# Kernel optimization log

Measured on AMD Instinct MI355X. Metric: run time of the kernel, lower is better.

## Reference

```python
import jax, jax.numpy as jnp
import numpy as np

BETA = 0.9
THR = 1.0
ALPHA = 2.0  # snntorch ATan surrogate default

@jax.custom_vjp
def spike(x):
    # Heaviside spike with ATan surrogate gradient (snntorch default)
    return (x > 0).astype(x.dtype)

def _spike_fwd(x):
    return spike(x), x

def _spike_bwd(x, g):
    grad = (ALPHA / 2.0) / (1.0 + (jnp.pi / 2.0 * ALPHA * x) ** 2)
    return (g * grad,)

spike.defvjp(_spike_fwd, _spike_bwd)

def setup_inputs() -> dict:
    key = jax.random.key(0)
    k1, k2, k3 = jax.random.split(key, 3)
    T, B, NI, NH, NO = 250, 256, 700, 1024, 20
    input_spikes = (jax.random.uniform(k1, (T, B, NI)) < 0.1).astype(jnp.float32)
    W1 = jax.random.normal(k2, (NH, NI), dtype=jnp.float32) / np.float32(np.sqrt(NI))
    W2 = jax.random.normal(k3, (NO, NH), dtype=jnp.float32) / np.float32(np.sqrt(NH))
    return {"input_spikes": input_spikes, "W1": W1, "W2": W2}

def reference(input_spikes, W1, W2):
    # fc1 over all timesteps in one GEMM: [T,B,NI] x [NH,NI] -> [T,B,NH]
    cur1 = jnp.einsum('tbi,hi->tbh', input_spikes, W1)

    # snntorch Leaky (reset_mechanism='subtract'):
    #   reset = detach(heaviside(mem_prev - thr))
    #   mem   = beta*mem_prev + cur - reset*thr
    #   spk   = heaviside(mem - thr)
    def lif_step(mem, c):
        reset = jax.lax.stop_gradient(spike(mem - THR))
        mem = BETA * mem + c - reset * THR
        spk = spike(mem - THR)
        return mem, spk

    mem0 = jnp.zeros(cur1.shape[1:], cur1.dtype)
    _, spk1 = jax.lax.scan(lif_step, mem0, cur1)  # [T,B,NH]

    # fc2 over all timesteps: [T,B,NH] x [NO,NH] -> [T,B,NO]
    cur2 = jnp.einsum('tbh,oh->tbo', spk1, W2)

    # Readout: Leaky with reset_mechanism='none' -> mem = beta*mem + cur
    def ro_step(mem, c):
        mem = BETA * mem + c
        return mem, mem

    m0 = jnp.zeros(cur2.shape[1:], cur2.dtype)
    _, mem_out_rec = jax.lax.scan(ro_step, m0, cur2)  # [T,B,NO]

    out_rec = jax.nn.softmax(mem_out_rec, axis=2)  # torch softmax dim=1 on [B,NO]
    return mem_out_rec, out_rec
```

## Files before the change

kernel.cpp:

```cpp
#include <hip/hip_runtime.h>
#include <hip/hip_bf16.h>
#include <cstdint>

#define T_STEPS 250
#define BATCH   256
#define NI      700
#define NH      1024
#define NO      20
#define BETAF   0.9f
#define KPAD    704
#define KT_N    22
#define KCAT    2112

typedef __attribute__((ext_vector_type(8))) short bf16x8;
typedef __attribute__((ext_vector_type(4))) float f32x4;

static __device__ __forceinline__ unsigned short f2bu(float x) {
    union { __hip_bfloat16 h; unsigned short u; } c;
    c.h = __float2bfloat16(x);
    return c.u;
}
static __device__ __forceinline__ float b2f(unsigned short u) {
    union { __hip_bfloat16 h; unsigned short u; } c;
    c.u = u;
    return __bfloat162float(c.h);
}

__global__ __launch_bounds__(256) void k0_init(const float* __restrict__ W1,
                                               const float* __restrict__ W2,
                                               float* __restrict__ W2T,
                                               float* __restrict__ mem1,
                                               unsigned short* __restrict__ Bcat) {
    int idx = blockIdx.x * 256 + threadIdx.x;
    if (idx < BATCH * NH) mem1[idx] = 0.f;
    if (idx < NH * NO) {
        int h = idx / NO, o = idx % NO;
        W2T[idx] = W2[o * NH + h];
    }
    if (idx < NH * KPAD) {
        int n = idx / KPAD, k = idx % KPAD;
        float w = (k < NI) ? W1[n * NI + k] : 0.f;
        unsigned short hu = f2bu(w);
        float r1 = w - b2f(hu);
        unsigned short mu = f2bu(r1);
        float r2 = r1 - b2f(mu);
        unsigned short lu = f2bu(r2);
        unsigned short* row = Bcat + (size_t)n * KCAT + k;
        row[0]        = hu;
        row[KPAD]     = mu;
        row[2 * KPAD] = lu;
    }
}

__global__ __launch_bounds__(256) void k1_cvt(const float* __restrict__ A,
                                              unsigned short* __restrict__ Abf,
                                              int rows) {
    int idx = blockIdx.x * 256 + threadIdx.x;
    int r = idx / 176, q = idx - r * 176;
    if (r >= rows) return;
    int k = q * 4;
    ushort4 o = make_ushort4(0, 0, 0, 0);
    if (k < NI) {
        float4 v = *(const float4*)(A + (size_t)r * NI + k);
        o.x = f2bu(v.x); o.y = f2bu(v.y); o.z = f2bu(v.z); o.w = f2bu(v.w);
    }
    *(ushort4*)(Abf + (size_t)r * KPAD + k) = o;
}

__global__ __launch_bounds__(256) void k2_fc1(const unsigned short* __restrict__ Abf,
                                              const unsigned short* __restrict__ Bcat,
                                              float* __restrict__ C) {
    __shared__ unsigned short As[128 * 32];
    __shared__ unsigned short Bs[3][128 * 32];
    const int tid  = threadIdx.x;
    const int lane = tid & 63;
    const int wv   = tid >> 6;

    int nwg = gridDim.x, bid = blockIdx.x, w;
    if ((nwg & 7) == 0) w = (bid & 7) * (nwg >> 3) + (bid >> 3);
    else                w = bid;
    const int brow = (w >> 3) * 128;
    const int bn   = (w & 7) * 128;
    const int wm   = (wv >> 1) * 64;
    const int wn   = (wv & 1) * 64;

    f32x4 acc[4][4];
#pragma unroll
    for (int i = 0; i < 4; ++i)
#pragma unroll
        for (int j = 0; j < 4; ++j) acc[i][j] = (f32x4){0.f, 0.f, 0.f, 0.f};

    auto stage = [&](const unsigned short* gbase, int rstride, int kcol,
                     unsigned short* lds) {
#pragma unroll
        for (int j = 0; j < 2; ++j) {
            int c   = wv * 128 + j * 64 + lane;
            int row = c >> 2;
            int lk  = ((c & 3) ^ ((row >> 1) & 3)) * 8;
            const unsigned short* src = gbase + (size_t)row * rstride + kcol + lk;
            __builtin_amdgcn_global_load_lds(
                (const __attribute__((address_space(1))) void*)src,
                (__attribute__((address_space(3))) void*)(lds + (wv * 128 + j * 64) * 8),
                16, 0, 0);
        }
    };

    const unsigned short* Ab = Abf + (size_t)brow * KPAD;
    const unsigned short* Bb = Bcat + (size_t)bn * KCAT;

    const int frow = lane & 15;
    const int fsl  = (((lane >> 4) & 3) ^ ((frow >> 1) & 3)) * 8;

    for (int kt = 0; kt < KT_N; ++kt) {
        stage(Ab, KPAD, kt * 32, As);
#pragma unroll
        for (int s = 0; s < 3; ++s)
            stage(Bb, KCAT, s * KPAD + kt * 32, Bs[s]);
        __syncthreads();

        bf16x8 a[4];
#pragma unroll
        for (int i = 0; i < 4; ++i)
            a[i] = *(const bf16x8*)&As[(wm + i * 16 + frow) * 32 + fsl];
#pragma unroll
        for (int s = 0; s < 3; ++s) {
#pragma unroll
            for (int j = 0; j < 4; ++j) {
                bf16x8 b = *(const bf16x8*)&Bs[s][(wn + j * 16 + frow) * 32 + fsl];
#pragma unroll
                for (int i = 0; i < 4; ++i)
                    acc[i][j] = __builtin_amdgcn_mfma_f32_16x16x32_bf16(a[i], b, acc[i][j], 0, 0, 0);
            }
        }
        __syncthreads();
    }

#pragma unroll
    for (int i = 0; i < 4; ++i) {
#pragma unroll
        for (int j = 0; j < 4; ++j) {
            int col  = bn + wn + j * 16 + (lane & 15);
            int row0 = brow + wm + i * 16 + ((lane >> 4) << 2);
#pragma unroll
            for (int q = 0; q < 4; ++q)
                C[(size_t)(row0 + q) * NH + col] = acc[i][j][q];
        }
    }
}

__global__ __launch_bounds__(256) void k3_lif(const float* __restrict__ cur1,
                                              float* __restrict__ mem1,
                                              unsigned long long* __restrict__ bits,
                                              int TC) {
    const int b    = blockIdx.x >> 1;
    const int half = blockIdx.x & 1;
    const int wv   = threadIdx.x >> 6;
    const int lane = threadIdx.x & 63;
    const int h    = half * 512 + wv * 128 + lane * 2;
    const size_t S = (size_t)BATCH * NH;
    const float* p = cur1 + (size_t)b * NH + h;
    unsigned long long* bp = bits + (size_t)b * 16 + (half * 4 + wv) * 2;
    const bool lead = lane == 0;

    float2 mm = *(const float2*)(mem1 + b * NH + h);
    float m0 = mm.x, m1 = mm.y;

    auto ld = [&](int t) -> float2 {
        int tt = t < TC ? t : TC - 1;
        return *(const float2*)(p + (size_t)tt * S);
    };

#define K3_STEP(cv, t)                                                         \
    {                                                                          \
        float r0 = (m0 > 1.f) ? 1.f : 0.f;                                     \
        m0 = fmaf(BETAF, m0, (cv).x) - r0;                                     \
        float r1 = (m1 > 1.f) ? 1.f : 0.f;                                     \
        m1 = fmaf(BETAF, m1, (cv).y) - r1;                                     \
        unsigned long long w0 = __ballot(m0 > 1.f);                            \
        unsigned long long w1 = __ballot(m1 > 1.f);                            \
        if (lead) {                                                            \
            ulonglong2 v; v.x = w0; v.y = w1;                                  \
            *(ulonglong2*)(bp + (size_t)(t) * (BATCH * 16)) = v;               \
        }                                                                      \
    }

    float2 c0 = ld(0), c1 = ld(1), c2 = ld(2), c3 = ld(3);
    int tc = 0;
    for (; tc + 4 <= TC; tc += 4) {
        K3_STEP(c0, tc + 0); c0 = ld(tc + 4);
        K3_STEP(c1, tc + 1); c1 = ld(tc + 5);
        K3_STEP(c2, tc + 2); c2 = ld(tc + 6);
        K3_STEP(c3, tc + 3); c3 = ld(tc + 7);
    }
    for (; tc < TC; ++tc) { float2 c = ld(tc); K3_STEP(c, tc); }
#undef K3_STEP
    float2 mo; mo.x = m0; mo.y = m1;
    *(float2*)(mem1 + b * NH + h) = mo;
}

__global__ __launch_bounds__(256) void k4_fc2(const unsigned long long* __restrict__ bits,
                                              const float* __restrict__ W2T,
                                              float* __restrict__ cur2) {
    int row  = blockIdx.x * 4 + (threadIdx.x >> 6);
    int lane = threadIdx.x & 63;
    bool act = lane < NO;
    unsigned long long mv = (lane < 16) ? bits[(size_t)row * 16 + lane] : 0ULL;
    const float* W = W2T + (act ? lane : 0);
    float p0 = 0.f, p1 = 0.f;
#pragma unroll
    for (int i = 0; i < 16; ++i) {
        unsigned long long m = __shfl(mv, i);
        int base = (i >> 1) * 128 + (i & 1);
        while (m) {
            int  b0 = __ffsll(m) - 1;            m &= m - 1;
            bool v1 = m != 0;
            int  b1 = v1 ? __ffsll(m) - 1 : 0;   m &= m - 1;
            float w0 = W[(base + 2 * b0) * NO];
            float w1 = W[(base + 2 * b1) * NO];
            p0 += w0;
            p1 += v1 ? w1 : 0.f;
        }
    }
    if (act) cur2[(size_t)row * NO + lane] = p0 + p1;
}

__global__ __launch_bounds__(64) void k5_readout(const float* __restrict__ cur2,
                                                 float* __restrict__ out_mem,
                                                 float* __restrict__ out_sm) {
    int b = blockIdx.x * 2 + (threadIdx.x >> 5);
    int o = threadIdx.x & 31;
    bool act = o < NO;
    const float* p = cur2 + (size_t)b * NO + (act ? o : 0);
    float mem = 0.f;
    float nxt = p[0];
    for (int t = 0; t < T_STEPS; ++t) {
        float c = nxt;
        if (t + 1 < T_STEPS) nxt = p[(size_t)(t + 1) * BATCH * NO];
        mem = fmaf(BETAF, mem, c);
        float e = act ? __expf(mem) : 0.f;
        float s = e;
#pragma unroll
        for (int off = 16; off; off >>= 1) s += __shfl_xor(s, off, 32);
        if (act) {
            int base = (t * BATCH + b) * NO;
            out_mem[base + o] = mem;
            out_sm[base + o] = __fdividef(e, s);
        }
    }
}

extern "C" void kernel_launch(void* const* d_in, const int* in_sizes, int n_in,
                              void* d_out, int out_size, void* d_ws, size_t ws_size,
                              hipStream_t stream) {
    const float* spikes = (const float*)d_in[0];
    const float* W1     = (const float*)d_in[1];
    const float* W2     = (const float*)d_in[2];
    float* out_mem = (float*)d_out;
    float* out_sm  = out_mem + (size_t)T_STEPS * BATCH * NO;

    char* ws = (char*)d_ws;
    size_t off = 0;
    auto alloc = [&](size_t bytes) -> char* {
        off = (off + 255) & ~(size_t)255;
        char* p = ws + off;
        off += bytes;
        return p;
    };
    float*          W2T  = (float*)alloc((size_t)NH * NO * 4);
    float*          mem1 = (float*)alloc((size_t)BATCH * NH * 4);
    float*          cur2 = (float*)alloc((size_t)T_STEPS * BATCH * NO * 4);
    unsigned short* Bcat = (unsigned short*)alloc((size_t)NH * KCAT * 2);

    size_t fixed = (off + 255) & ~(size_t)255;
    size_t rem = ws_size > fixed ? ws_size - fixed : 0;
    size_t per_t = (size_t)BATCH * NH * 4 + (size_t)BATCH * KPAD * 2
                 + (size_t)BATCH * 16 * 8 + 768;
    int TC = (int)(rem / per_t);
    if (TC > T_STEPS) TC = T_STEPS;
    if (TC < 1) TC = 1;
    float*              cur1 = (float*)alloc((size_t)TC * BATCH * NH * 4);
    unsigned short*     Abf  = (unsigned short*)alloc((size_t)TC * BATCH * KPAD * 2);
    unsigned long long* bits = (unsigned long long*)alloc((size_t)TC * BATCH * 16 * 8);

    k0_init<<<(NH * KPAD + 255) / 256, 256, 0, stream>>>(W1, W2, W2T, mem1, Bcat);

    for (int t0 = 0; t0 < T_STEPS; t0 += TC) {
        int tc = T_STEPS - t0 < TC ? T_STEPS - t0 : TC;
        int rows = tc * BATCH;
        k1_cvt<<<(rows * 176 + 255) / 256, 256, 0, stream>>>(
            spikes + (size_t)t0 * BATCH * NI, Abf, rows);
        int nwg = (rows / 128) * 8;
        k2_fc1<<<nwg, 256, 0, stream>>>(Abf, Bcat, cur1);
        k3_lif<<<512, 256, 0, stream>>>(cur1, mem1, bits, tc);
        k4_fc2<<<rows / 4, 256, 0, stream>>>(bits, W2T, cur2 + (size_t)t0 * BATCH * NO);
    }

    k5_readout<<<128, 64, 0, stream>>>(cur2, out_mem, out_sm);
}
```

Before: 521.0 us.

## Enlarge fc1 GEMM tile to 256x256 with double-buffered LDS pipelining

The fc1 GEMM moves from 128x128 tiles with 4 waves to 256x256 tiles with 8 waves. LDS is now double-buffered, so global-to-LDS loads for the next K step are issued while MFMAs run on the current buffer. The work is split into interleaved stages with s_setprio and barriers. This aims to raise data reuse and hide load latency, at the cost of more LDS, more registers and fewer workgroups.

```diff
diff --git a/kernel.cpp b/kernel.cpp
--- a/kernel.cpp
+++ b/kernel.cpp
@@ -67,83 +67,129 @@
     *(ushort4*)(Abf + (size_t)r * KPAD + k) = o;
 }
 
-__global__ __launch_bounds__(256) void k2_fc1(const unsigned short* __restrict__ Abf,
+__global__ __launch_bounds__(512) void k2_fc1(const unsigned short* __restrict__ Abf,
                                               const unsigned short* __restrict__ Bcat,
                                               float* __restrict__ C) {
-    __shared__ unsigned short As[128 * 32];
-    __shared__ unsigned short Bs[3][128 * 32];
+    __shared__ unsigned short As[2][256 * 32];
+    __shared__ unsigned short Bs[2][3][256 * 32];
     const int tid  = threadIdx.x;
     const int lane = tid & 63;
     const int wv   = tid >> 6;
+    const int wr   = wv >> 2;
+    const int wc   = wv & 3;
 
     int nwg = gridDim.x, bid = blockIdx.x, w;
     if ((nwg & 7) == 0) w = (bid & 7) * (nwg >> 3) + (bid >> 3);
     else                w = bid;
-    const int brow = (w >> 3) * 128;
-    const int bn   = (w & 7) * 128;
-    const int wm   = (wv >> 1) * 64;
-    const int wn   = (wv & 1) * 64;
-
-    f32x4 acc[4][4];
-#pragma unroll
-    for (int i = 0; i < 4; ++i)
-#pragma unroll
-        for (int j = 0; j < 4; ++j) acc[i][j] = (f32x4){0.f, 0.f, 0.f, 0.f};
-
-    auto stage = [&](const unsigned short* gbase, int rstride, int kcol,
-                     unsigned short* lds) {
-#pragma unroll
-        for (int j = 0; j < 2; ++j) {
-            int c   = wv * 128 + j * 64 + lane;
-            int row = c >> 2;
-            int lk  = ((c & 3) ^ ((row >> 1) & 3)) * 8;
-            const unsigned short* src = gbase + (size_t)row * rstride + kcol + lk;
-            __builtin_amdgcn_global_load_lds(
-                (const __attribute__((address_space(1))) void*)src,
-                (__attribute__((address_space(3))) void*)(lds + (wv * 128 + j * 64) * 8),
-                16, 0, 0);
-        }
-    };
+    const int brow = (w >> 2) * 256;
+    const int bn   = (w & 3) * 256;
+
+    f32x4 acc[8][4];
+#pragma unroll
+    for (int f = 0; f < 8; ++f)
+#pragma unroll
+        for (int j = 0; j < 4; ++j) acc[f][j] = (f32x4){0.f, 0.f, 0.f, 0.f};
 
     const unsigned short* Ab = Abf + (size_t)brow * KPAD;
     const unsigned short* Bb = Bcat + (size_t)bn * KCAT;
 
+    auto stageHalf = [&](const unsigned short* gbase, int rstride, int kcol,
+                         int h, unsigned short* tile) {
+        int c   = h * 512 + wv * 64 + lane;
+        int row = c >> 2;
+        int lk  = ((c & 3) ^ ((row >> 1) & 3)) * 8;
+        const unsigned short* src = gbase + (size_t)row * rstride + kcol + lk;
+        __builtin_amdgcn_global_load_lds(
+            (const __attribute__((address_space(1))) void*)src,
+            (__attribute__((address_space(3))) void*)(tile + (size_t)(h * 512 + wv * 64) * 8),
+            16, 0, 0);
+    };
+
     const int frow = lane & 15;
     const int fsl  = (((lane >> 4) & 3) ^ ((frow >> 1) & 3)) * 8;
 
+    bf16x8 a[4], b0[4], b1[4], b2[4];
+    auto loadA = [&](const unsigned short* Ac, int mh) {
+#pragma unroll
+        for (int i = 0; i < 4; ++i)
+            a[i] = *(const bf16x8*)&Ac[(wr * 128 + mh * 64 + i * 16 + frow) * 32 + fsl];
+    };
+    auto loadB = [&](const unsigned short* Bc, bf16x8* b) {
+#pragma unroll
+        for (int j = 0; j < 4; ++j)
+            b[j] = *(const bf16x8*)&Bc[(wc * 64 + j * 16 + frow) * 32 + fsl];
+    };
+    auto mm = [&](int mh, const bf16x8* b) {
+        __builtin_amdgcn_s_setprio(1);
+#pragma unroll
+        for (int j = 0; j < 4; ++j)
+#pragma unroll
+            for (int i = 0; i < 4; ++i)
+                acc[mh * 4 + i][j] = __builtin_amdgcn_mfma_f32_16x16x32_bf16(
+                    a[i], b[j], acc[mh * 4 + i][j], 0, 0, 0);
+        __builtin_amdgcn_s_setprio(0);
+    };
+
+    stageHalf(Ab, KPAD, 0, 0, As[0]);
+    stageHalf(Ab, KPAD, 0, 1, As[0]);
+#pragma unroll
+    for (int s = 0; s < 3; ++s) {
+        stageHalf(Bb, KCAT, s * KPAD, 0, Bs[0][s]);
+        stageHalf(Bb, KCAT, s * KPAD, 1, Bs[0][s]);
+    }
+    asm volatile("s_waitcnt vmcnt(0)" ::: "memory");
+    __builtin_amdgcn_s_barrier();
+
     for (int kt = 0; kt < KT_N; ++kt) {
-        stage(Ab, KPAD, kt * 32, As);
-#pragma unroll
-        for (int s = 0; s < 3; ++s)
-            stage(Bb, KCAT, s * KPAD + kt * 32, Bs[s]);
-        __syncthreads();
-
-        bf16x8 a[4];
-#pragma unroll
-        for (int i = 0; i < 4; ++i)
-            a[i] = *(const bf16x8*)&As[(wm + i * 16 + frow) * 32 + fsl];
-#pragma unroll
-        for (int s = 0; s < 3; ++s) {
-#pragma unroll
-            for (int j = 0; j < 4; ++j) {
-                bf16x8 b = *(const bf16x8*)&Bs[s][(wn + j * 16 + frow) * 32 + fsl];
-#pragma unroll
-                for (int i = 0; i < 4; ++i)
-                    acc[i][j] = __builtin_amdgcn_mfma_f32_16x16x32_bf16(a[i], b, acc[i][j], 0, 0, 0);
-            }
-        }
-        __syncthreads();
-    }
-
-#pragma unroll
-    for (int i = 0; i < 4; ++i) {
+        const int buf = kt & 1;
+        const unsigned short* Ac = As[buf];
+        const unsigned short* B0 = Bs[buf][0];
+        const unsigned short* B1 = Bs[buf][1];
+        const unsigned short* B2 = Bs[buf][2];
+        const bool st = (kt + 1 < KT_N);
+        const int kc = (kt + 1) * 32;
+
+        if (st) { stageHalf(Ab, KPAD, kc, 0, As[buf ^ 1]);
+                  stageHalf(Ab, KPAD, kc, 1, As[buf ^ 1]); }
+        loadA(Ac, 0);
+        loadB(B0, b0);
+        __builtin_amdgcn_s_barrier();
+        mm(0, b0);
+        __builtin_amdgcn_s_barrier();
+        if (st) { stageHalf(Bb, KCAT, kc, 0, Bs[buf ^ 1][0]);
+                  stageHalf(Bb, KCAT, kc, 1, Bs[buf ^ 1][0]); }
+        loadB(B1, b1);
+        __builtin_amdgcn_s_barrier();
+        mm(0, b1);
+        __builtin_amdgcn_s_barrier();
+        if (st) { stageHalf(Bb, KCAT, KPAD + kc, 0, Bs[buf ^ 1][1]);
+                  stageHalf(Bb, KCAT, KPAD + kc, 1, Bs[buf ^ 1][1]); }
+        loadB(B2, b2);
+        __builtin_amdgcn_s_barrier();
+        mm(0, b2);
+        __builtin_amdgcn_s_barrier();
+        if (st) { stageHalf(Bb, KCAT, 2 * KPAD + kc, 0, Bs[buf ^ 1][2]);
+                  stageHalf(Bb, KCAT, 2 * KPAD + kc, 1, Bs[buf ^ 1][2]); }
+        loadA(Ac, 1);
+        __builtin_amdgcn_s_barrier();
+        mm(1, b0);
+        __builtin_amdgcn_s_barrier();
+        mm(1, b1);
+        __builtin_amdgcn_s_barrier();
+        mm(1, b2);
+        if (st) asm volatile("s_waitcnt vmcnt(0)" ::: "memory");
+        __builtin_amdgcn_s_barrier();
+    }
+
+#pragma unroll
+    for (int f = 0; f < 8; ++f) {
 #pragma unroll
         for (int j = 0; j < 4; ++j) {
-            int col  = bn + wn + j * 16 + (lane & 15);
-            int row0 = brow + wm + i * 16 + ((lane >> 4) << 2);
+            int col  = bn + wc * 64 + j * 16 + (lane & 15);
+            int row0 = brow + wr * 128 + f * 16 + ((lane >> 4) << 2);
 #pragma unroll
             for (int q = 0; q < 4; ++q)
-                C[(size_t)(row0 + q) * NH + col] = acc[i][j][q];
+                C[(size_t)(row0 + q) * NH + col] = acc[f][j][q];
         }
     }
 }
@@ -289,8 +335,8 @@
         int rows = tc * BATCH;
         k1_cvt<<<(rows * 176 + 255) / 256, 256, 0, stream>>>(
             spikes + (size_t)t0 * BATCH * NI, Abf, rows);
-        int nwg = (rows / 128) * 8;
-        k2_fc1<<<nwg, 256, 0, stream>>>(Abf, Bcat, cur1);
+        int nwg = (rows / 256) * 4;
+        k2_fc1<<<nwg, 512, 0, stream>>>(Abf, Bcat, cur1);
         k3_lif<<<512, 256, 0, stream>>>(cur1, mem1, bits, tc);
         k4_fc2<<<rows / 4, 256, 0, stream>>>(bits, W2T, cur2 + (size_t)t0 * BATCH * NO);
     }
```

Result: no change. 520.7 us (-0.1%).

## Double-buffer fc1 GEMM tiles with 512-thread 256x128 blocks and split-phase prefetch

Applied to the files above, without the earlier changes.

Rewrites the fc1 GEMM kernel to use 512-thread workgroups that each compute a 256x128 output tile, doubling the A-tile height. LDS tiles for A and the three concatenated B slices are now double-buffered, and the next k-tile's loads are issued in stages between MFMA phases using explicit vmcnt waits and raw barriers. s_setprio is raised around the MFMA bursts. The aim is to hide global-to-LDS latency behind compute and get more reuse per loaded tile, at the cost of more LDS per block and more fragile hand-tuned wait counts.

```diff
diff --git a/kernel.cpp b/kernel.cpp
--- a/kernel.cpp
+++ b/kernel.cpp
@@ -67,22 +67,22 @@
     *(ushort4*)(Abf + (size_t)r * KPAD + k) = o;
 }
 
-__global__ __launch_bounds__(256) void k2_fc1(const unsigned short* __restrict__ Abf,
-                                              const unsigned short* __restrict__ Bcat,
-                                              float* __restrict__ C) {
-    __shared__ unsigned short As[128 * 32];
-    __shared__ unsigned short Bs[3][128 * 32];
+__global__ __launch_bounds__(512, 4) void k2_fc1(const unsigned short* __restrict__ Abf,
+                                                 const unsigned short* __restrict__ Bcat,
+                                                 float* __restrict__ C) {
+    __shared__ unsigned short As[2][256 * 32];
+    __shared__ unsigned short Bs[2][3][128 * 32];
     const int tid  = threadIdx.x;
     const int lane = tid & 63;
     const int wv   = tid >> 6;
+    const int wr   = wv >> 1;
+    const int wc   = wv & 1;
 
     int nwg = gridDim.x, bid = blockIdx.x, w;
     if ((nwg & 7) == 0) w = (bid & 7) * (nwg >> 3) + (bid >> 3);
     else                w = bid;
-    const int brow = (w >> 3) * 128;
+    const int brow = (w >> 3) * 256;
     const int bn   = (w & 7) * 128;
-    const int wm   = (wv >> 1) * 64;
-    const int wn   = (wv & 1) * 64;
 
     f32x4 acc[4][4];
 #pragma unroll
@@ -90,57 +90,99 @@
 #pragma unroll
         for (int j = 0; j < 4; ++j) acc[i][j] = (f32x4){0.f, 0.f, 0.f, 0.f};
 
-    auto stage = [&](const unsigned short* gbase, int rstride, int kcol,
-                     unsigned short* lds) {
+    const unsigned short* Ab = Abf + (size_t)brow * KPAD;
+    const unsigned short* Bb = Bcat + (size_t)bn * KCAT;
+
+    auto stageA = [&](int kcol, unsigned short* tile) {
 #pragma unroll
         for (int j = 0; j < 2; ++j) {
-            int c   = wv * 128 + j * 64 + lane;
+            int c   = j * 512 + wv * 64 + lane;
             int row = c >> 2;
             int lk  = ((c & 3) ^ ((row >> 1) & 3)) * 8;
-            const unsigned short* src = gbase + (size_t)row * rstride + kcol + lk;
+            const unsigned short* src = Ab + (size_t)row * KPAD + kcol + lk;
             __builtin_amdgcn_global_load_lds(
                 (const __attribute__((address_space(1))) void*)src,
-                (__attribute__((address_space(3))) void*)(lds + (wv * 128 + j * 64) * 8),
+                (__attribute__((address_space(3))) void*)(tile + (size_t)(j * 512 + wv * 64) * 8),
                 16, 0, 0);
         }
     };
-
-    const unsigned short* Ab = Abf + (size_t)brow * KPAD;
-    const unsigned short* Bb = Bcat + (size_t)bn * KCAT;
+    auto stageB = [&](int kcol, unsigned short* tile) {
+        int c   = wv * 64 + lane;
+        int row = c >> 2;
+        int lk  = ((c & 3) ^ ((row >> 1) & 3)) * 8;
+        const unsigned short* src = Bb + (size_t)row * KCAT + kcol + lk;
+        __builtin_amdgcn_global_load_lds(
+            (const __attribute__((address_space(1))) void*)src,
+            (__attribute__((address_space(3))) void*)(tile + (size_t)(wv * 64) * 8),
+            16, 0, 0);
+    };
 
     const int frow = lane & 15;
     const int fsl  = (((lane >> 4) & 3) ^ ((frow >> 1) & 3)) * 8;
 
+    bf16x8 a[4], b[4];
+    auto loadA = [&](const unsigned short* Ac) {
+#pragma unroll
+        for (int i = 0; i < 4; ++i)
+            a[i] = *(const bf16x8*)&Ac[(wr * 64 + i * 16 + frow) * 32 + fsl];
+    };
+    auto loadB = [&](const unsigned short* Bc) {
+#pragma unroll
+        for (int j = 0; j < 4; ++j)
+            b[j] = *(const bf16x8*)&Bc[(wc * 64 + j * 16 + frow) * 32 + fsl];
+    };
+    auto mm = [&]() {
+        __builtin_amdgcn_s_setprio(1);
+#pragma unroll
+        for (int j = 0; j < 4; ++j)
+#pragma unroll
+            for (int i = 0; i < 4; ++i)
+                acc[i][j] = __builtin_amdgcn_mfma_f32_16x16x32_bf16(
+                    a[i], b[j], acc[i][j], 0, 0, 0);
+        __builtin_amdgcn_s_setprio(0);
+    };
+
+    stageA(0, As[0]);
+#pragma unroll
+    for (int s = 0; s < 3; ++s) stageB(s * KPAD, Bs[0][s]);
+    asm volatile("s_waitcnt vmcnt(0)" ::: "memory");
+    __builtin_amdgcn_s_barrier();
+
     for (int kt = 0; kt < KT_N; ++kt) {
-        stage(Ab, KPAD, kt * 32, As);
-#pragma unroll
-        for (int s = 0; s < 3; ++s)
-            stage(Bb, KCAT, s * KPAD + kt * 32, Bs[s]);
-        __syncthreads();
-
-        bf16x8 a[4];
-#pragma unroll
-        for (int i = 0; i < 4; ++i)
-            a[i] = *(const bf16x8*)&As[(wm + i * 16 + frow) * 32 + fsl];
-#pragma unroll
-        for (int s = 0; s < 3; ++s) {
-#pragma unroll
-            for (int j = 0; j < 4; ++j) {
-                bf16x8 b = *(const bf16x8*)&Bs[s][(wn + j * 16 + frow) * 32 + fsl];
-#pragma unroll
-                for (int i = 0; i < 4; ++i)
-                    acc[i][j] = __builtin_amdgcn_mfma_f32_16x16x32_bf16(a[i], b, acc[i][j], 0, 0, 0);
-            }
-        }
-        __syncthreads();
+        const int buf = kt & 1;
+        const bool st = (kt + 1 < KT_N);
+        const int kc = (kt + 1) * 32;
+
+        asm volatile("s_waitcnt vmcnt(2)" ::: "memory");
+        if (st) stageA(kc, As[buf ^ 1]);
+        __builtin_amdgcn_s_barrier();
+        loadA(As[buf]);
+        loadB(Bs[buf][0]);
+        mm();
+        __builtin_amdgcn_s_barrier();
+        if (st) asm volatile("s_waitcnt vmcnt(3)" ::: "memory");
+        else    asm volatile("s_waitcnt vmcnt(1)" ::: "memory");
+        if (st) stageB(kc, Bs[buf ^ 1][0]);
+        __builtin_amdgcn_s_barrier();
+        loadB(Bs[buf][1]);
+        mm();
+        __builtin_amdgcn_s_barrier();
+        if (st) asm volatile("s_waitcnt vmcnt(3)" ::: "memory");
+        else    asm volatile("s_waitcnt vmcnt(0)" ::: "memory");
+        if (st) { stageB(KPAD + kc, Bs[buf ^ 1][1]);
+                  stageB(2 * KPAD + kc, Bs[buf ^ 1][2]); }
+        __builtin_amdgcn_s_barrier();
+        loadB(Bs[buf][2]);
+        mm();
+        __builtin_amdgcn_s_barrier();
     }
 
 #pragma unroll
     for (int i = 0; i < 4; ++i) {
 #pragma unroll
         for (int j = 0; j < 4; ++j) {
-            int col  = bn + wn + j * 16 + (lane & 15);
-            int row0 = brow + wm + i * 16 + ((lane >> 4) << 2);
+            int col  = bn + wc * 64 + j * 16 + (lane & 15);
+            int row0 = brow + wr * 64 + i * 16 + ((lane >> 4) << 2);
 #pragma unroll
             for (int q = 0; q < 4; ++q)
                 C[(size_t)(row0 + q) * NH + col] = acc[i][j][q];
@@ -289,8 +331,8 @@
         int rows = tc * BATCH;
         k1_cvt<<<(rows * 176 + 255) / 256, 256, 0, stream>>>(
             spikes + (size_t)t0 * BATCH * NI, Abf, rows);
-        int nwg = (rows / 128) * 8;
-        k2_fc1<<<nwg, 256, 0, stream>>>(Abf, Bcat, cur1);
+        int nwg = (rows / 256) * 8;
+        k2_fc1<<<nwg, 512, 0, stream>>>(Abf, Bcat, cur1);
         k3_lif<<<512, 256, 0, stream>>>(cur1, mem1, bits, tc);
         k4_fc2<<<rows / 4, 256, 0, stream>>>(bits, W2T, cur2 + (size_t)t0 * BATCH * NO);
     }
```

Result: faster. 509.6 us (-2.2%).
